# Performance work log

Measured on AMD Instinct MI355X. Metric: run time of the kernel, lower is better.

Reference implementation:

```python
import jax, jax.numpy as jnp
import numpy as np

B, T, D = 2, 2048, 1024
H, KVH = 16, 4
HD = D // H            # 64
HALF = HD // 2         # 32
DFF = 4096
KW = 15
EPS = 1e-6


def zcrms(x, scale):
    # zero-centred RMSNorm: (1 + scale) * x / rms(x)
    rms = jnp.sqrt(jnp.mean(jnp.square(x.astype(jnp.float32)), axis=-1, keepdims=True) + EPS)
    return ((1.0 + scale) * x / rms).astype(x.dtype)


def apply_rope(x, cos, sin):
    # x: [B, H, T, HD]; cos/sin: [T, HALF]
    c = cos[None, None, :, :]
    s = sin[None, None, :, :]
    x1, x2 = x[..., :HALF], x[..., HALF:]
    return jnp.concatenate([x1 * c - x2 * s, x2 * c + x1 * s], axis=-1)


def setup_inputs() -> dict:
    key = jax.random.key(0)
    ks = jax.random.split(key, 20)
    std = 0.02
    inp = {
        "x": jax.random.normal(ks[0], (B, T, D), jnp.float32),
        "mask": jnp.ones((1, 1, T, T), dtype=bool),
        "cos": jnp.cos(jnp.arange(T, dtype=jnp.float32)[:, None]
                       * (10000.0 ** (-jnp.arange(HALF, dtype=jnp.float32) / HALF))[None, :]),
        "sin": jnp.sin(jnp.arange(T, dtype=jnp.float32)[:, None]
                       * (10000.0 ** (-jnp.arange(HALF, dtype=jnp.float32) / HALF))[None, :]),
        # attention
        "attn_norm_scale": jax.random.normal(ks[1], (D,), jnp.float32) * std,
        "q_kernel": jax.random.normal(ks[2], (D, D), jnp.float32) * std,
        "k_kernel": jax.random.normal(ks[3], (D, KVH * HD), jnp.float32) * std,
        "v_kernel": jax.random.normal(ks[4], (D, KVH * HD), jnp.float32) * std,
        "q_norm_scale": jax.random.normal(ks[5], (HD,), jnp.float32) * std,
        "k_norm_scale": jax.random.normal(ks[6], (HD,), jnp.float32) * std,
        "o_kernel": jax.random.normal(ks[7], (D, D), jnp.float32) * std,
        # conv module
        "conv_norm_scale": jax.random.normal(ks[8], (D,), jnp.float32) * std,
        "pw_up_kernel": jax.random.normal(ks[9], (D, 2 * D), jnp.float32) * std,
        "dw_kernel": jax.random.normal(ks[10], (KW, 1, D), jnp.float32) * std,
        "conv_inner_norm_scale": jax.random.normal(ks[11], (D,), jnp.float32) * std,
        "pw_down_kernel": jax.random.normal(ks[12], (D, D), jnp.float32) * std,
        # ffn
        "ffn_norm_scale": jax.random.normal(ks[13], (D,), jnp.float32) * std,
        "gate_kernel": jax.random.normal(ks[14], (D, DFF), jnp.float32) * std,
        "up_kernel": jax.random.normal(ks[15], (D, DFF), jnp.float32) * std,
        "down_kernel": jax.random.normal(ks[16], (DFF, D), jnp.float32) * std,
    }
    return inp


def reference(x, mask, cos, sin, attn_norm_scale, q_kernel, k_kernel, v_kernel,
              q_norm_scale, k_norm_scale, o_kernel, conv_norm_scale, pw_up_kernel,
              dw_kernel, conv_inner_norm_scale, pw_down_kernel, ffn_norm_scale,
              gate_kernel, up_kernel, down_kernel):
    # ---- pre-norm self-attention (GQA + QK-RMSNorm + RoPE) ----
    h = zcrms(x, attn_norm_scale)
    q = (h @ q_kernel).reshape(B, T, H, HD).transpose(0, 2, 1, 3)      # [B,H,T,HD]
    k = (h @ k_kernel).reshape(B, T, KVH, HD).transpose(0, 2, 1, 3)    # [B,KVH,T,HD]
    v = (h @ v_kernel).reshape(B, T, KVH, HD).transpose(0, 2, 1, 3)
    q = zcrms(q, q_norm_scale)
    k = zcrms(k, k_norm_scale)
    rep = H // KVH
    k = jnp.repeat(k, rep, axis=1)
    v = jnp.repeat(v, rep, axis=1)
    q = apply_rope(q, cos, sin)
    k = apply_rope(k, cos, sin)
    scale = jnp.sqrt(jnp.float32(HD))
    aw = jnp.einsum('bhqd,bhkd->bhqk', q, k) / scale
    aw = jnp.where(mask, aw, jnp.finfo(aw.dtype).min)
    aw = jax.nn.softmax(aw, axis=-1)
    attn = jnp.einsum('bhqk,bhkd->bhqd', aw, v).transpose(0, 2, 1, 3).reshape(B, T, D)
    x = x + attn @ o_kernel

    # ---- conformer conv module: pw_up -> GLU -> depthwise conv -> norm -> pw_down ----
    h = zcrms(x, conv_norm_scale)
    u = h @ pw_up_kernel
    u1, u2 = jnp.split(u, 2, axis=-1)
    g = u1 * jax.nn.sigmoid(u2)                                        # [B,T,D]
    c = jax.lax.conv_general_dilated(
        g, dw_kernel, window_strides=(1,), padding='SAME',
        feature_group_count=D, dimension_numbers=('NWC', 'WIO', 'NWC'))
    c = zcrms(c, conv_inner_norm_scale)
    x = x + c @ pw_down_kernel

    # ---- gated FFN with drelu activation ----
    h = zcrms(x, ffn_norm_scale)
    ff = jax.nn.relu(h @ gate_kernel) * jax.nn.relu(h @ up_kernel)
    x = x + ff @ down_kernel
    return x
```

## Files before the change

kernel.cpp:

```cpp
#include <hip/hip_runtime.h>


#define TT   2048
#define NTOK 4096

typedef __attribute__((ext_vector_type(8))) short short8;
typedef __attribute__((ext_vector_type(4))) float floatx4;

__device__ __forceinline__ unsigned short f2bf(float f) {
  unsigned int u = __float_as_uint(f);
  u = (u + 0x7fffu + ((u >> 16) & 1u)) >> 16;
  return (unsigned short)u;
}
__device__ __forceinline__ float bf2f(unsigned short s) {
  return __uint_as_float(((unsigned int)s) << 16);
}

__device__ __forceinline__ void glds16(const void* g, void* lds_base) {
  __builtin_amdgcn_global_load_lds(
      (const __attribute__((address_space(1))) void*)g,
      (__attribute__((address_space(3))) void*)lds_base, 16, 0, 0);
}

struct WJobs {
  const float* src[9];
  unsigned short* dst[9];
  int K[9], M[9], pm[9];
  int start[10];
};

__global__ __launch_bounds__(256) void wconv_all_kernel(WJobs tab) {
  int b = blockIdx.x;
  int j = 0;
  while (b >= tab.start[j + 1]) j++;
  int t = b - tab.start[j];
  const float* src = tab.src[j];
  unsigned short* dst = tab.dst[j];
  int K = tab.K[j], M = tab.M[j], pm = tab.pm[j];
  int mt = M >> 5;
  int m0 = (t % mt) * 32, k0 = (t / mt) * 32;
  int rowbase;
  if (pm == 0)      rowbase = m0;
  else if (pm == 1) rowbase = ((m0 & 1023) >> 5) * 64 + (m0 >> 10) * 32;
  else if (pm == 2) rowbase = (m0 >> 5) * 64;
  else              rowbase = (m0 >> 5) * 64 + 32;
  __shared__ float tile[32][33];
  int tx = threadIdx.x & 31, ty = threadIdx.x >> 5;
  for (int r = ty; r < 32; r += 8)
    tile[r][tx] = src[(size_t)(k0 + r) * M + m0 + tx];
  __syncthreads();
  for (int r = ty; r < 32; r += 8)
    dst[(size_t)(rowbase + r) * K + k0 + tx] = f2bf(tile[tx][r]);
}

template <bool BF16IN>
__global__ __launch_bounds__(256) void rmsnorm_kernel(
    const void* __restrict__ xin, const float* __restrict__ scale,
    unsigned short* __restrict__ out) {
  int t = blockIdx.x, tid = threadIdx.x;
  float xv[4];
  if (BF16IN) {
    ushort4 u = ((const ushort4*)((const unsigned short*)xin + (size_t)t * 1024))[tid];
    xv[0] = bf2f(u.x); xv[1] = bf2f(u.y); xv[2] = bf2f(u.z); xv[3] = bf2f(u.w);
  } else {
    float4 u = ((const float4*)((const float*)xin + (size_t)t * 1024))[tid];
    xv[0] = u.x; xv[1] = u.y; xv[2] = u.z; xv[3] = u.w;
  }
  float ss = xv[0] * xv[0] + xv[1] * xv[1] + xv[2] * xv[2] + xv[3] * xv[3];
#pragma unroll
  for (int off = 32; off > 0; off >>= 1) ss += __shfl_down(ss, off);
  __shared__ float red[4];
  if ((tid & 63) == 0) red[tid >> 6] = ss;
  __syncthreads();
  float rinv = rsqrtf((red[0] + red[1] + red[2] + red[3]) * (1.0f / 1024.0f) + 1e-6f);
  float4 sv = ((const float4*)scale)[tid];
  ushort4 o;
  o.x = f2bf((1.0f + sv.x) * xv[0] * rinv);
  o.y = f2bf((1.0f + sv.y) * xv[1] * rinv);
  o.z = f2bf((1.0f + sv.z) * xv[2] * rinv);
  o.w = f2bf((1.0f + sv.w) * xv[3] * rinv);
  ((ushort4*)(out + (size_t)t * 1024))[tid] = o;
}

template <int BN, int FUSE, int OUT, int RES>
__global__ __launch_bounds__(256, 2) void gemm_bt_kernel(
    const unsigned short* __restrict__ A, const unsigned short* __restrict__ Bt,
    void* __restrict__ Cout, const void* __restrict__ resid, int K, int M) {
  constexpr int NI = BN / 32;
  __shared__ __align__(16) unsigned short As[128 * 64];
  __shared__ __align__(16) unsigned short Bs[BN * 64];
  const int tid = threadIdx.x;
  const int wid = tid >> 6, lane = tid & 63;
  const int quad = lane >> 4, l16 = lane & 15;
  const int wm = (wid >> 1) * 64, wn = (wid & 1) * (BN / 2);
  const int row0 = blockIdx.y * 128;
  const int col0 = blockIdx.x * BN;

  floatx4 acc[4][NI];
#pragma unroll
  for (int mi = 0; mi < 4; mi++)
#pragma unroll
    for (int ni = 0; ni < NI; ni++) acc[mi][ni] = (floatx4){0.f, 0.f, 0.f, 0.f};

  const unsigned short* Ag = A + (size_t)row0 * K;
  const unsigned short* Bg = Bt + (size_t)col0 * K;

  for (int k0 = 0; k0 < K; k0 += 64) {
#pragma unroll
    for (int j = 0; j < 4; j++) {
      int ci = tid + j * 256;
      int r = ci >> 3, c = (ci & 7) ^ (r & 7);
      glds16(Ag + (size_t)r * K + k0 + c * 8, &As[(wid * 64 + j * 256) * 8]);
    }
#pragma unroll
    for (int j = 0; j < BN / 32; j++) {
      int ci = tid + j * 256;
      int r = ci >> 3, c = (ci & 7) ^ (r & 7);
      glds16(Bg + (size_t)r * K + k0 + c * 8, &Bs[(wid * 64 + j * 256) * 8]);
    }
    __syncthreads();
#pragma unroll
    for (int kk = 0; kk < 64; kk += 32) {
      short8 a[4], b[NI];
#pragma unroll
      for (int mi = 0; mi < 4; mi++) {
        int r = wm + mi * 16 + l16;
        a[mi] = *(const short8*)&As[r * 64 + (((kk >> 3) + quad) ^ (r & 7)) * 8];
      }
#pragma unroll
      for (int ni = 0; ni < NI; ni++) {
        int r = wn + ni * 16 + l16;
        b[ni] = *(const short8*)&Bs[r * 64 + (((kk >> 3) + quad) ^ (r & 7)) * 8];
      }
#pragma unroll
      for (int mi = 0; mi < 4; mi++)
#pragma unroll
        for (int ni = 0; ni < NI; ni++)
          acc[mi][ni] = __builtin_amdgcn_mfma_f32_16x16x32_bf16(a[mi], b[ni], acc[mi][ni], 0, 0, 0);
    }
    __syncthreads();
  }

  if (FUSE == 0) {
#pragma unroll
    for (int mi = 0; mi < 4; mi++) {
#pragma unroll
      for (int reg = 0; reg < 4; reg++) {
        int grow = row0 + wm + mi * 16 + quad * 4 + reg;
#pragma unroll
        for (int ni = 0; ni < NI; ni++) {
          int gcol = col0 + wn + ni * 16 + l16;
          float v = acc[mi][ni][reg];
          if (RES == 1) v += ((const float*)resid)[(size_t)grow * M + gcol];
          if (RES == 2) v += bf2f(((const unsigned short*)resid)[(size_t)grow * M + gcol]);
          if (OUT == 1) ((unsigned short*)Cout)[(size_t)grow * M + gcol] = f2bf(v);
          else          ((float*)Cout)[(size_t)grow * M + gcol] = v;
        }
      }
    }
  } else {
    const int group = (col0 + wn) >> 6;
    const int MW = M >> 1;
#pragma unroll
    for (int mi = 0; mi < 4; mi++) {
#pragma unroll
      for (int reg = 0; reg < 4; reg++) {
        int grow = row0 + wm + mi * 16 + quad * 4 + reg;
#pragma unroll
        for (int ni = 0; ni < NI / 2; ni++) {
          int f = group * 32 + ni * 16 + l16;
          float a = acc[mi][ni][reg], b = acc[mi][ni + NI / 2][reg];
          float v;
          if (FUSE == 1) v = a / (1.0f + __expf(-b));
          else           v = fmaxf(a, 0.f) * fmaxf(b, 0.f);
          ((unsigned short*)Cout)[(size_t)grow * MW + f] = f2bf(v);
        }
      }
    }
  }
}

#define QSCALE 0.180336880111f

__global__ __launch_bounds__(256) void qknorm_rope_kernel(
    const unsigned short* __restrict__ qkv, const float* __restrict__ cosb,
    const float* __restrict__ sinb, const float* __restrict__ qns,
    const float* __restrict__ kns, unsigned short* __restrict__ qb,
    unsigned short* __restrict__ kb) {
  int tok = blockIdx.x;
  int tid = threadIdx.x, w = tid >> 6, lane = tid & 63;
  int pos = tok & (TT - 1);
  int half = lane & 31;
  float c = cosb[pos * 32 + half], s = sinb[pos * 32 + half];
  const unsigned short* row = qkv + (size_t)tok * 1536;
  for (int hr = w; hr < 20; hr += 4) {
    float v = bf2f(row[hr * 64 + lane]);
    float ss = v * v;
#pragma unroll
    for (int off = 32; off > 0; off >>= 1) ss += __shfl_xor(ss, off);
    float rinv = rsqrtf(ss * (1.0f / 64.0f) + 1e-6f);
    float sc = (hr < 16) ? qns[lane] : kns[lane];
    float nv = (1.0f + sc) * v * rinv;
    float partner = __shfl_xor(nv, 32);
    float outv = (lane < 32) ? (nv * c - partner * s) : (nv * c + partner * s);
    if (hr < 16) qb[(size_t)tok * 1024 + hr * 64 + lane] = f2bf(outv * QSCALE);
    else         kb[(size_t)tok * 256 + (hr - 16) * 64 + lane] = f2bf(outv);
  }
}

__global__ __launch_bounds__(256) void vtrans_kernel(
    const unsigned short* __restrict__ qkv, unsigned short* __restrict__ vt) {
  __shared__ unsigned short t[64 * 65];
  int ktile = blockIdx.x;
  int g = blockIdx.y;
  int bi = g >> 2, kvh = g & 3;
  int tid = threadIdx.x;
#pragma unroll
  for (int j = 0; j < 2; j++) {
    int ci = tid + j * 256;
    int r = ci >> 3, c8 = (ci & 7) * 8;
    union { uint4 v; unsigned short u[8]; } uu;
    uu.v = *(const uint4*)(qkv + (size_t)(bi * TT + ktile * 64 + r) * 1536 +
                           1280 + kvh * 64 + c8);
#pragma unroll
    for (int e = 0; e < 8; e++) t[r * 65 + c8 + e] = uu.u[e];
  }
  __syncthreads();
#pragma unroll
  for (int j = 0; j < 2; j++) {
    int ci = tid + j * 256;
    int d = ci >> 3, c8 = (ci & 7) * 8;
    union { uint4 v; unsigned short u[8]; } uu;
#pragma unroll
    for (int e = 0; e < 8; e++) uu.u[e] = t[(c8 + e) * 65 + d];
    *(uint4*)(vt + ((size_t)(g * 64 + d)) * TT + ktile * 64 + c8) = uu.v;
  }
}

__global__ __launch_bounds__(512) void flash_kernel(
    const unsigned short* __restrict__ qb, const unsigned short* __restrict__ kb,
    const unsigned short* __restrict__ vt, unsigned short* __restrict__ ob) {
  const int qt = blockIdx.x;
  const int bh = blockIdx.y;
  const int bi = bh >> 4, h = bh & 15, kvh = h >> 2;
  const int tid = threadIdx.x, w = tid >> 6, lane = tid & 63;
  const int quad = lane >> 4, l16 = lane & 15;

  __shared__ __align__(16) unsigned short Ks[2][64 * 64];
  __shared__ __align__(16) unsigned short Vs[2][64 * 64];
  __shared__ __align__(16) unsigned short Ps[256 * 64];

  const unsigned short* qsrc = qb + ((size_t)(bi * TT + qt * 256)) * 1024 + h * 64;
  short8 qf[2][2];
#pragma unroll
  for (int af = 0; af < 2; af++) {
    const unsigned short* qr = qsrc + (size_t)(w * 32 + af * 16 + l16) * 1024;
    qf[af][0] = *(const short8*)(qr + quad * 8);
    qf[af][1] = *(const short8*)(qr + 32 + quad * 8);
  }

  const unsigned short* kbase = kb + ((size_t)(bi * TT)) * 256 + kvh * 64;
  const unsigned short* vbase = vt + ((size_t)(bi * 4 + kvh)) * (64 * TT);

  floatx4 oacc[2][4];
  floatx4 lacc[2];
#pragma unroll
  for (int af = 0; af < 2; af++) {
    lacc[af] = (floatx4){0.f, 0.f, 0.f, 0.f};
#pragma unroll
    for (int di = 0; di < 4; di++) oacc[af][di] = (floatx4){0.f, 0.f, 0.f, 0.f};
  }
  const short8 ones = (short8){0x3F80, 0x3F80, 0x3F80, 0x3F80,
                               0x3F80, 0x3F80, 0x3F80, 0x3F80};

  {
    int r = tid >> 3, c = (tid & 7) ^ (r & 7);
    glds16(kbase + (size_t)r * 256 + c * 8, &Ks[0][w * 512]);
    glds16(vbase + (size_t)r * TT + c * 8, &Vs[0][w * 512]);
  }

  for (int kt = 0; kt < 32; kt++) {
    const int buf = kt & 1;
    __syncthreads();
    if (kt < 31) {
      int r = tid >> 3, c = (tid & 7) ^ (r & 7);
      glds16(kbase + (size_t)((kt + 1) * 64 + r) * 256 + c * 8, &Ks[buf ^ 1][w * 512]);
      glds16(vbase + (size_t)r * TT + (kt + 1) * 64 + c * 8, &Vs[buf ^ 1][w * 512]);
    }

    short8 kf[4][2];
#pragma unroll
    for (int ni = 0; ni < 4; ni++) {
      int rb = ni * 16 + l16;
      kf[ni][0] = *(const short8*)&Ks[buf][rb * 64 + ((quad ^ (rb & 7)) * 8)];
      kf[ni][1] = *(const short8*)&Ks[buf][rb * 64 + (((4 + quad) ^ (rb & 7)) * 8)];
    }
#pragma unroll
    for (int af = 0; af < 2; af++) {
#pragma unroll
      for (int ni = 0; ni < 4; ni++) {
        floatx4 s = (floatx4){0.f, 0.f, 0.f, 0.f};
        s = __builtin_amdgcn_mfma_f32_16x16x32_bf16(qf[af][0], kf[ni][0], s, 0, 0, 0);
        s = __builtin_amdgcn_mfma_f32_16x16x32_bf16(qf[af][1], kf[ni][1], s, 0, 0, 0);
#pragma unroll
        for (int r = 0; r < 4; r++) {
          int rr = w * 32 + af * 16 + quad * 4 + r;
          int ch = (ni * 2 + (l16 >> 3)) ^ (rr & 7);
          Ps[rr * 64 + ch * 8 + (l16 & 7)] =
              (unsigned short)(__float_as_uint(__builtin_amdgcn_exp2f(s[r])) >> 16);
        }
      }
    }
    short8 vf[4][2];
#pragma unroll
    for (int di = 0; di < 4; di++) {
      int rb = di * 16 + l16;
      vf[di][0] = *(const short8*)&Vs[buf][rb * 64 + ((quad ^ (rb & 7)) * 8)];
      vf[di][1] = *(const short8*)&Vs[buf][rb * 64 + (((4 + quad) ^ (rb & 7)) * 8)];
    }
#pragma unroll
    for (int af = 0; af < 2; af++) {
      const int rr = w * 32 + af * 16 + l16;
      short8 pa0 = *(const short8*)&Ps[rr * 64 + ((quad ^ (rr & 7)) * 8)];
      short8 pa1 = *(const short8*)&Ps[rr * 64 + (((4 + quad) ^ (rr & 7)) * 8)];
      lacc[af] = __builtin_amdgcn_mfma_f32_16x16x32_bf16(pa0, ones, lacc[af], 0, 0, 0);
      lacc[af] = __builtin_amdgcn_mfma_f32_16x16x32_bf16(pa1, ones, lacc[af], 0, 0, 0);
#pragma unroll
      for (int di = 0; di < 4; di++) {
        oacc[af][di] = __builtin_amdgcn_mfma_f32_16x16x32_bf16(pa0, vf[di][0], oacc[af][di], 0, 0, 0);
        oacc[af][di] = __builtin_amdgcn_mfma_f32_16x16x32_bf16(pa1, vf[di][1], oacc[af][di], 0, 0, 0);
      }
    }
  }

  unsigned short* obase = ob + ((size_t)(bi * TT + qt * 256)) * 1024 + h * 64;
#pragma unroll
  for (int af = 0; af < 2; af++) {
    float rl[4];
#pragma unroll
    for (int r = 0; r < 4; r++) rl[r] = 1.0f / lacc[af][r];
#pragma unroll
    for (int di = 0; di < 4; di++)
#pragma unroll
      for (int r = 0; r < 4; r++) {
        int qrow = w * 32 + af * 16 + quad * 4 + r;
        obase[(size_t)qrow * 1024 + di * 16 + l16] = f2bf(oacc[af][di][r] * rl[r]);
      }
  }
}

__global__ __launch_bounds__(256) void convnorm_kernel(
    const unsigned short* __restrict__ g, const float* __restrict__ dw,
    const float* __restrict__ scale, unsigned short* __restrict__ out) {
  int tok = blockIdx.x;
  int bi = tok >> 11, pos = tok & (TT - 1);
  int tid = threadIdx.x, c0 = tid * 4;
  float a0 = 0.f, a1 = 0.f, a2 = 0.f, a3 = 0.f;
#pragma unroll
  for (int wk = 0; wk < 15; wk++) {
    int pp = pos + wk - 7;
    if (pp < 0 || pp >= TT) continue;
    ushort4 gv = *(const ushort4*)(g + ((size_t)(bi * TT + pp)) * 1024 + c0);
    float4 kv = *(const float4*)(dw + wk * 1024 + c0);
    a0 += bf2f(gv.x) * kv.x;
    a1 += bf2f(gv.y) * kv.y;
    a2 += bf2f(gv.z) * kv.z;
    a3 += bf2f(gv.w) * kv.w;
  }
  float ss = a0 * a0 + a1 * a1 + a2 * a2 + a3 * a3;
#pragma unroll
  for (int off = 32; off > 0; off >>= 1) ss += __shfl_down(ss, off);
  __shared__ float red[4];
  if ((tid & 63) == 0) red[tid >> 6] = ss;
  __syncthreads();
  float rinv = rsqrtf((red[0] + red[1] + red[2] + red[3]) * (1.0f / 1024.0f) + 1e-6f);
  float4 sv = *(const float4*)(scale + c0);
  ushort4 o;
  o.x = f2bf((1.0f + sv.x) * a0 * rinv);
  o.y = f2bf((1.0f + sv.y) * a1 * rinv);
  o.z = f2bf((1.0f + sv.z) * a2 * rinv);
  o.w = f2bf((1.0f + sv.w) * a3 * rinv);
  *(ushort4*)(out + (size_t)tok * 1024 + c0) = o;
}

extern "C" void kernel_launch(void* const* d_in, const int* in_sizes, int n_in,
                              void* d_out, int out_size, void* d_ws, size_t ws_size,
                              hipStream_t stream) {
  const float* x        = (const float*)d_in[0];
  const float* cosb     = (const float*)d_in[2];
  const float* sinb     = (const float*)d_in[3];
  const float* attn_ns  = (const float*)d_in[4];
  const float* qkern    = (const float*)d_in[5];
  const float* kkern    = (const float*)d_in[6];
  const float* vkern    = (const float*)d_in[7];
  const float* qns      = (const float*)d_in[8];
  const float* kns      = (const float*)d_in[9];
  const float* okern    = (const float*)d_in[10];
  const float* conv_ns  = (const float*)d_in[11];
  const float* pwupk    = (const float*)d_in[12];
  const float* dwk      = (const float*)d_in[13];
  const float* convi_ns = (const float*)d_in[14];
  const float* pwdnk    = (const float*)d_in[15];
  const float* ffn_ns   = (const float*)d_in[16];
  const float* gatek    = (const float*)d_in[17];
  const float* upk      = (const float*)d_in[18];
  const float* downk    = (const float*)d_in[19];
  float* out = (float*)d_out;
  char* ws = (char*)d_ws;

  const size_t O_QKVT = 0;
  const size_t O_OT   = O_QKVT + (size_t)1536 * 1024 * 2;
  const size_t O_UPT  = O_OT   + (size_t)1024 * 1024 * 2;
  const size_t O_DNT  = O_UPT  + (size_t)2048 * 1024 * 2;
  const size_t O_GUT  = O_DNT  + (size_t)1024 * 1024 * 2;
  const size_t O_DWNT = O_GUT  + (size_t)8192 * 1024 * 2;
  const size_t O_H    = O_DWNT + (size_t)4096 * 1024 * 2;
  const size_t O_BIG1 = O_H    + (size_t)4096 * 1024 * 2;
  const size_t O_QB   = O_BIG1 + (size_t)4096 * 8192 * 2;
  const size_t O_KB   = O_QB   + (size_t)4096 * 1024 * 2;
  const size_t O_VT   = O_KB   + (size_t)4096 * 256 * 2;
  const size_t O_ECN  = O_VT   + (size_t)8 * 64 * 2048 * 2;
  const size_t O_X1   = O_ECN  + (size_t)4096 * 1024 * 2;
  const size_t O_X2   = O_X1   + (size_t)4096 * 1024 * 2;
  const size_t O_BIG2 = O_X2   + (size_t)4096 * 1024 * 2;

  unsigned short* qkvT = (unsigned short*)(ws + O_QKVT);
  unsigned short* oT   = (unsigned short*)(ws + O_OT);
  unsigned short* upT  = (unsigned short*)(ws + O_UPT);
  unsigned short* dnT  = (unsigned short*)(ws + O_DNT);
  unsigned short* guT  = (unsigned short*)(ws + O_GUT);
  unsigned short* dwT  = (unsigned short*)(ws + O_DWNT);
  unsigned short* hbuf = (unsigned short*)(ws + O_H);
  unsigned short* big1u = (unsigned short*)(ws + O_BIG1);
  unsigned short* qbuf = (unsigned short*)(ws + O_QB);
  unsigned short* kbuf = (unsigned short*)(ws + O_KB);
  unsigned short* vtb  = (unsigned short*)(ws + O_VT);
  unsigned short* ecn  = (unsigned short*)(ws + O_ECN);
  unsigned short* x1b  = (unsigned short*)(ws + O_X1);
  unsigned short* x2b  = (unsigned short*)(ws + O_X2);
  unsigned short* big2 = (unsigned short*)(ws + O_BIG2);

  WJobs tab;
  tab.src[0] = qkern;  tab.dst[0] = qkvT;                       tab.K[0] = 1024; tab.M[0] = 1024; tab.pm[0] = 0;
  tab.src[1] = kkern;  tab.dst[1] = qkvT + (size_t)1024 * 1024; tab.K[1] = 1024; tab.M[1] = 256;  tab.pm[1] = 0;
  tab.src[2] = vkern;  tab.dst[2] = qkvT + (size_t)1280 * 1024; tab.K[2] = 1024; tab.M[2] = 256;  tab.pm[2] = 0;
  tab.src[3] = okern;  tab.dst[3] = oT;                         tab.K[3] = 1024; tab.M[3] = 1024; tab.pm[3] = 0;
  tab.src[4] = pwupk;  tab.dst[4] = upT;                        tab.K[4] = 1024; tab.M[4] = 2048; tab.pm[4] = 1;
  tab.src[5] = pwdnk;  tab.dst[5] = dnT;                        tab.K[5] = 1024; tab.M[5] = 1024; tab.pm[5] = 0;
  tab.src[6] = gatek;  tab.dst[6] = guT;                        tab.K[6] = 1024; tab.M[6] = 4096; tab.pm[6] = 2;
  tab.src[7] = upk;    tab.dst[7] = guT;                        tab.K[7] = 1024; tab.M[7] = 4096; tab.pm[7] = 3;
  tab.src[8] = downk;  tab.dst[8] = dwT;                        tab.K[8] = 4096; tab.M[8] = 1024; tab.pm[8] = 0;
  tab.start[0] = 0;
  for (int i = 0; i < 9; i++)
    tab.start[i + 1] = tab.start[i] + (tab.M[i] >> 5) * (tab.K[i] >> 5);
  wconv_all_kernel<<<tab.start[9], 256, 0, stream>>>(tab);

  rmsnorm_kernel<false><<<NTOK, 256, 0, stream>>>(x, attn_ns, hbuf);
  gemm_bt_kernel<128, 0, 1, 0><<<dim3(12, 32), 256, 0, stream>>>(
      hbuf, qkvT, big1u, nullptr, 1024, 1536);
  qknorm_rope_kernel<<<NTOK, 256, 0, stream>>>(big1u, cosb, sinb, qns, kns,
                                               qbuf, kbuf);
  vtrans_kernel<<<dim3(32, 8), 256, 0, stream>>>(big1u, vtb);
  flash_kernel<<<dim3(8, 32), 512, 0, stream>>>(qbuf, kbuf, vtb, ecn);
  gemm_bt_kernel<64, 0, 1, 1><<<dim3(16, 32), 256, 0, stream>>>(
      ecn, oT, x1b, x, 1024, 1024);

  rmsnorm_kernel<true><<<NTOK, 256, 0, stream>>>(x1b, conv_ns, hbuf);
  gemm_bt_kernel<128, 1, 1, 0><<<dim3(16, 32), 256, 0, stream>>>(
      hbuf, upT, big2, nullptr, 1024, 2048);
  convnorm_kernel<<<NTOK, 256, 0, stream>>>(big2, dwk, convi_ns, ecn);
  gemm_bt_kernel<64, 0, 1, 2><<<dim3(16, 32), 256, 0, stream>>>(
      ecn, dnT, x2b, x1b, 1024, 1024);

  rmsnorm_kernel<true><<<NTOK, 256, 0, stream>>>(x2b, ffn_ns, hbuf);
  gemm_bt_kernel<128, 2, 1, 0><<<dim3(64, 32), 256, 0, stream>>>(
      hbuf, guT, big1u, nullptr, 1024, 8192);
  gemm_bt_kernel<64, 0, 0, 2><<<dim3(16, 32), 256, 0, stream>>>(
      big1u, dwT, out, x2b, 4096, 1024);
}
```

Before: 488.6 us.

## Swizzle GEMM block order for L2 reuse and vectorize flash P stores

GEMM blocks are remapped into 8x8 supertiles when gridDim.x is a multiple of 8, so concurrently running workgroups share A and B tiles in cache. In the flash kernel the QK^T MFMA operands are swapped so each lane holds four consecutive keys. That lets the bf16 probabilities go to LDS as a single 64-bit store instead of four scalar stores. GEMM template instances also become named wrapper kernels, mostly for profiling clarity. The remap assumes gridDim.y is 32 and adds a little index arithmetic.

```diff
diff --git a/kernel.cpp b/kernel.cpp
--- a/kernel.cpp
+++ b/kernel.cpp
@@ -83,7 +83,7 @@
 }
 
 template <int BN, int FUSE, int OUT, int RES>
-__global__ __launch_bounds__(256, 2) void gemm_bt_kernel(
+__device__ __forceinline__ void gemm_body(
     const unsigned short* __restrict__ A, const unsigned short* __restrict__ Bt,
     void* __restrict__ Cout, const void* __restrict__ resid, int K, int M) {
   constexpr int NI = BN / 32;
@@ -93,8 +93,16 @@
   const int wid = tid >> 6, lane = tid & 63;
   const int quad = lane >> 4, l16 = lane & 15;
   const int wm = (wid >> 1) * 64, wn = (wid & 1) * (BN / 2);
-  const int row0 = blockIdx.y * 128;
-  const int col0 = blockIdx.x * BN;
+
+  int bx = blockIdx.x, by = blockIdx.y;
+  if ((gridDim.x & 7) == 0) {
+    int pid = by * gridDim.x + bx;
+    int inb = pid & 63, pidp = pid >> 6;
+    by = (pidp & 3) * 8 + (inb & 7);
+    bx = (pidp >> 2) * 8 + (inb >> 3);
+  }
+  const int row0 = by * 128;
+  const int col0 = bx * BN;
 
   floatx4 acc[4][NI];
 #pragma unroll
@@ -178,6 +186,31 @@
       }
     }
   }
+}
+
+__global__ __launch_bounds__(256, 2) void gemm_qkv(
+    const unsigned short* A, const unsigned short* Bt, void* C, const void* r, int K, int M) {
+  gemm_body<128, 0, 1, 0>(A, Bt, C, r, K, M);
+}
+__global__ __launch_bounds__(256, 2) void gemm_oproj(
+    const unsigned short* A, const unsigned short* Bt, void* C, const void* r, int K, int M) {
+  gemm_body<64, 0, 1, 1>(A, Bt, C, r, K, M);
+}
+__global__ __launch_bounds__(256, 2) void gemm_glu(
+    const unsigned short* A, const unsigned short* Bt, void* C, const void* r, int K, int M) {
+  gemm_body<128, 1, 1, 0>(A, Bt, C, r, K, M);
+}
+__global__ __launch_bounds__(256, 2) void gemm_dn(
+    const unsigned short* A, const unsigned short* Bt, void* C, const void* r, int K, int M) {
+  gemm_body<64, 0, 1, 2>(A, Bt, C, r, K, M);
+}
+__global__ __launch_bounds__(256, 2) void gemm_gateup(
+    const unsigned short* A, const unsigned short* Bt, void* C, const void* r, int K, int M) {
+  gemm_body<128, 2, 1, 0>(A, Bt, C, r, K, M);
+}
+__global__ __launch_bounds__(256, 2) void gemm_ffdn(
+    const unsigned short* A, const unsigned short* Bt, void* C, const void* r, int K, int M) {
+  gemm_body<64, 0, 0, 2>(A, Bt, C, r, K, M);
 }
 
 #define QSCALE 0.180336880111f
@@ -297,18 +330,18 @@
     }
 #pragma unroll
     for (int af = 0; af < 2; af++) {
+      const int rr = w * 32 + af * 16 + l16;
 #pragma unroll
       for (int ni = 0; ni < 4; ni++) {
         floatx4 s = (floatx4){0.f, 0.f, 0.f, 0.f};
-        s = __builtin_amdgcn_mfma_f32_16x16x32_bf16(qf[af][0], kf[ni][0], s, 0, 0, 0);
-        s = __builtin_amdgcn_mfma_f32_16x16x32_bf16(qf[af][1], kf[ni][1], s, 0, 0, 0);
-#pragma unroll
-        for (int r = 0; r < 4; r++) {
-          int rr = w * 32 + af * 16 + quad * 4 + r;
-          int ch = (ni * 2 + (l16 >> 3)) ^ (rr & 7);
-          Ps[rr * 64 + ch * 8 + (l16 & 7)] =
-              (unsigned short)(__float_as_uint(__builtin_amdgcn_exp2f(s[r])) >> 16);
-        }
+        s = __builtin_amdgcn_mfma_f32_16x16x32_bf16(kf[ni][0], qf[af][0], s, 0, 0, 0);
+        s = __builtin_amdgcn_mfma_f32_16x16x32_bf16(kf[ni][1], qf[af][1], s, 0, 0, 0);
+        union { unsigned short u[4]; unsigned long long ull; } pk;
+#pragma unroll
+        for (int r = 0; r < 4; r++)
+          pk.u[r] = (unsigned short)(__float_as_uint(__builtin_amdgcn_exp2f(s[r])) >> 16);
+        int ch = (ni * 2 + (quad >> 1)) ^ (rr & 7);
+        *(unsigned long long*)&Ps[rr * 64 + ch * 8 + (quad & 1) * 4] = pk.ull;
       }
     }
     short8 vf[4][2];
@@ -456,25 +489,19 @@
   wconv_all_kernel<<<tab.start[9], 256, 0, stream>>>(tab);
 
   rmsnorm_kernel<false><<<NTOK, 256, 0, stream>>>(x, attn_ns, hbuf);
-  gemm_bt_kernel<128, 0, 1, 0><<<dim3(12, 32), 256, 0, stream>>>(
-      hbuf, qkvT, big1u, nullptr, 1024, 1536);
+  gemm_qkv<<<dim3(12, 32), 256, 0, stream>>>(hbuf, qkvT, big1u, nullptr, 1024, 1536);
   qknorm_rope_kernel<<<NTOK, 256, 0, stream>>>(big1u, cosb, sinb, qns, kns,
                                                qbuf, kbuf);
   vtrans_kernel<<<dim3(32, 8), 256, 0, stream>>>(big1u, vtb);
   flash_kernel<<<dim3(8, 32), 512, 0, stream>>>(qbuf, kbuf, vtb, ecn);
-  gemm_bt_kernel<64, 0, 1, 1><<<dim3(16, 32), 256, 0, stream>>>(
-      ecn, oT, x1b, x, 1024, 1024);
+  gemm_oproj<<<dim3(16, 32), 256, 0, stream>>>(ecn, oT, x1b, x, 1024, 1024);
 
   rmsnorm_kernel<true><<<NTOK, 256, 0, stream>>>(x1b, conv_ns, hbuf);
-  gemm_bt_kernel<128, 1, 1, 0><<<dim3(16, 32), 256, 0, stream>>>(
-      hbuf, upT, big2, nullptr, 1024, 2048);
+  gemm_glu<<<dim3(16, 32), 256, 0, stream>>>(hbuf, upT, big2, nullptr, 1024, 2048);
   convnorm_kernel<<<NTOK, 256, 0, stream>>>(big2, dwk, convi_ns, ecn);
-  gemm_bt_kernel<64, 0, 1, 2><<<dim3(16, 32), 256, 0, stream>>>(
-      ecn, dnT, x2b, x1b, 1024, 1024);
+  gemm_dn<<<dim3(16, 32), 256, 0, stream>>>(ecn, dnT, x2b, x1b, 1024, 1024);
 
   rmsnorm_kernel<true><<<NTOK, 256, 0, stream>>>(x2b, ffn_ns, hbuf);
-  gemm_bt_kernel<128, 2, 1, 0><<<dim3(64, 32), 256, 0, stream>>>(
-      hbuf, guT, big1u, nullptr, 1024, 8192);
-  gemm_bt_kernel<64, 0, 0, 2><<<dim3(16, 32), 256, 0, stream>>>(
-      big1u, dwT, out, x2b, 4096, 1024);
-}
+  gemm_gateup<<<dim3(64, 32), 256, 0, stream>>>(hbuf, guT, big1u, nullptr, 1024, 8192);
+  gemm_ffdn<<<dim3(16, 32), 256, 0, stream>>>(big1u, dwT, out, x2b, 4096, 1024);
+}
```

Result: no change. 484.8 us (-0.8%).
